# Optimization experiments

Measured on AMD Instinct MI355X. Metric: run time of the kernel, lower is better.

## Reference

```python
import jax, jax.numpy as jnp
import numpy as np


def setup_inputs() -> dict:
    key = jax.random.key(0)
    ks = jax.random.split(key, 13)
    B, W, C = 16, 2048, 512
    inp = {
        "X_sfr": jax.random.normal(ks[0], (B, W, C), dtype=jnp.float32),
        "adj_matrix": jax.random.normal(ks[1], (B, C, C), dtype=jnp.float32),
        "log_temp": jnp.zeros((1,), dtype=jnp.float32),
        "wq": jax.random.normal(ks[2], (1,), dtype=jnp.float32),
        "bq": jax.random.normal(ks[3], (1,), dtype=jnp.float32),
        "wk": jax.random.normal(ks[4], (1,), dtype=jnp.float32),
        "bk": jax.random.normal(ks[5], (1,), dtype=jnp.float32),
        "wv": jax.random.normal(ks[6], (1,), dtype=jnp.float32),
        "bv": jax.random.normal(ks[7], (1,), dtype=jnp.float32),
        "wmu": jax.random.normal(ks[8], (1,), dtype=jnp.float32),
        "bmu": jax.random.normal(ks[9], (1,), dtype=jnp.float32),
        "wsig": jax.random.normal(ks[10], (1,), dtype=jnp.float32),
        "bsig": jax.random.normal(ks[11], (1,), dtype=jnp.float32),
        "k1": 20,
        "k2": 30,
    }
    return inp


def reference(X_sfr, adj_matrix, log_temp, wq, bq, wk, bk, wv, bv, wmu, bmu, wsig, bsig, k1, k2):
    B, W, C = X_sfr.shape
    # spatial propagation: relu + in-degree normalize adjacency
    adj_nonneg = jnp.maximum(adj_matrix, 0.0)
    in_deg = jnp.clip(adj_nonneg.sum(axis=1, keepdims=True), 1e-4)  # [B,1,C]
    adj_norm = adj_nonneg / in_deg
    X_spatial = jnp.einsum('bwi,bij->bwj', X_sfr, adj_norm)  # [B,W,C]

    # static band mask over time: k1 <= |dt| <= k2, fallback to identity rows
    t = jnp.arange(W)
    delta = jnp.abs(t[None, :] - t[:, None])
    band = (delta >= k1) & (delta <= k2)  # [W,W]
    has_valid = band.any(axis=1)
    band = jnp.where(has_valid[:, None], band, jnp.eye(W, dtype=bool))

    # scalar (1->1) q/k/v projections on the temporal token
    temporal_token = X_spatial.mean(axis=2, keepdims=True)  # [B,W,1]
    q = wq * temporal_token + bq                            # [B,W,1]
    k = wk * temporal_token + bk                            # [B,W,1]
    v = wv * X_spatial + bv                                 # [B,W,C]

    temp = jax.nn.softplus(log_temp)[0] + 1e-4
    logits = jnp.matmul(q, jnp.swapaxes(k, 1, 2)) / temp    # [B,W,W] rank-1
    logits = jnp.where(band[None, :, :], logits, -1e9)
    attn = jax.nn.softmax(logits, axis=-1)
    attn = attn * band[None, :, :].astype(attn.dtype)
    attn = attn / (attn.sum(axis=-1, keepdims=True) + 1e-6)

    sacon_scalar = attn.sum(axis=-1, keepdims=True)         # [B,W,1]
    sacon = jnp.broadcast_to(sacon_scalar, (B, W, C))

    X_temporal = jnp.matmul(attn, v)                        # [B,W,C]
    X_fused = X_temporal + X_spatial

    mu = jnp.clip(wmu * X_fused + bmu, -20.0, 20.0)
    sigma_sq = jax.nn.softplus(wsig * X_fused + bsig) + 0.1
    return mu, sigma_sq, sacon
```

## Files before the change

### kernel.cpp

```cpp
#include <hip/hip_runtime.h>
#include <math.h>

#define B_ 16
#define W_ 2048
#define C_ 512

#define OFF_XB    0
#define OFF_BT    33554432
#define OFF_XSP   41943040
#define OFF_TT    75497472
#define OFF_CS    75628544

typedef short v8s __attribute__((ext_vector_type(8)));
typedef float v4f __attribute__((ext_vector_type(4)));
typedef float v2f __attribute__((ext_vector_type(2)));
typedef unsigned int u32;

__device__ __forceinline__ float softplus_fast(float x) {
    return fmaxf(x, 0.f) + __logf(1.f + __expf(-fabsf(x)));
}
__device__ __forceinline__ unsigned short f2bf(float x) {
    unsigned int u = __float_as_uint(x);
    unsigned int r = (u + 0x7FFFu + ((u >> 16) & 1u)) >> 16;
    return (unsigned short)r;
}
__device__ __forceinline__ float bf2f(unsigned int h) {
    return __uint_as_float(h << 16);
}
__device__ __forceinline__ void gload16(const ushort* g, ushort* l) {
    __builtin_amdgcn_global_load_lds(
        (const __attribute__((address_space(1))) u32*)(g),
        (__attribute__((address_space(3))) u32*)(l), 16, 0, 0);
}

__global__ __launch_bounds__(256) void colsum_k(const float* __restrict__ adj,
                                                float* __restrict__ cs) {
    __shared__ float red[8][32];
    const int b = blockIdx.z, j0 = blockIdx.x * 32, r0 = blockIdx.y * 128;
    const int tx = threadIdx.x & 31, ty = threadIdx.x >> 5;
    const float* src = adj + (size_t)b * C_ * C_;

    float s = 0.f;
#pragma unroll 4
    for (int it = 0; it < 16; it++)
        s += fmaxf(src[(size_t)(r0 + it * 8 + ty) * C_ + j0 + tx], 0.f);
    red[ty][tx] = s;
    __syncthreads();
    if (ty == 0) {
        float tot = red[0][tx] + red[1][tx] + red[2][tx] + red[3][tx]
                  + red[4][tx] + red[5][tx] + red[6][tx] + red[7][tx];
        atomicAdd(&cs[b * C_ + j0 + tx], tot);
    }
}

__global__ __launch_bounds__(256) void prep_bt(const float* __restrict__ adj,
                                               const float* __restrict__ cs,
                                               ushort* __restrict__ Bt) {
    __shared__ float t[64][65];
    __shared__ float invs[64];
    const int b = blockIdx.z;
    const int i0 = blockIdx.x * 64;
    const int j0 = blockIdx.y * 64;
    const int tid = threadIdx.x;
    const int tx = tid & 15, ty = tid >> 4;

    if (tid < 64) invs[tid] = 1.f / fmaxf(cs[b * C_ + j0 + tid], 1e-4f);

#pragma unroll
    for (int p = 0; p < 4; p++) {
        const int iy = ty + p * 16;
        const float4 v = *(const float4*)&adj[((size_t)b * C_ + (i0 + iy)) * C_ + j0 + tx * 4];
        t[iy][tx * 4 + 0] = fmaxf(v.x, 0.f);
        t[iy][tx * 4 + 1] = fmaxf(v.y, 0.f);
        t[iy][tx * 4 + 2] = fmaxf(v.z, 0.f);
        t[iy][tx * 4 + 3] = fmaxf(v.w, 0.f);
    }
    __syncthreads();

    const int jj = tid >> 2;
    const int i4 = (tid & 3) * 16;
    const float iv = invs[jj];
    v8s o0, o1;
#pragma unroll
    for (int k = 0; k < 8; k++) o0[k] = (short)f2bf(t[i4 + k][jj] * iv);
#pragma unroll
    for (int k = 0; k < 8; k++) o1[k] = (short)f2bf(t[i4 + 8 + k][jj] * iv);
    ushort* dst = &Bt[(size_t)b * C_ * C_ + (size_t)(j0 + jj) * C_ + i0 + i4];
    *(v8s*)dst       = o0;
    *(v8s*)(dst + 8) = o1;
}

__global__ void convertA(const float* __restrict__ X, ushort* __restrict__ Xb) {
    int idx = blockIdx.x * 256 + threadIdx.x;
    float4 v = ((const float4*)X)[idx];
    ushort4 o;
    o.x = f2bf(v.x); o.y = f2bf(v.y); o.z = f2bf(v.z); o.w = f2bf(v.w);
    ((ushort4*)Xb)[idx] = o;
}

__global__ __launch_bounds__(256) void gemm_mfma(const ushort* __restrict__ Xb,
                                                 const ushort* __restrict__ Bt,
                                                 ushort* __restrict__ Xsp,
                                                 float* __restrict__ tt) {
    __shared__ ushort As[128 * 32];
    __shared__ ushort Bs[128 * 32];
    const int b  = blockIdx.z;
    const int m0 = blockIdx.y * 128;
    const int n0 = blockIdx.x * 128;
    const int tid  = threadIdx.x;
    const int wave = tid >> 6, lane = tid & 63;
    const int quad = lane >> 4, l16 = lane & 15;
    const int mw = (wave & 1) * 64, nw = (wave >> 1) * 64;

    const ushort* Ag = Xb + (size_t)b * W_ * C_ + (size_t)m0 * C_;
    const ushort* Bg = Bt + (size_t)b * C_ * C_ + (size_t)n0 * C_;

    const int sm = tid >> 2;
    const int sk = (tid & 3) * 8;

    v4f acc[4][4];
#pragma unroll
    for (int mt = 0; mt < 4; mt++)
#pragma unroll
        for (int nt = 0; nt < 4; nt++)
            acc[mt][nt] = (v4f){0.f, 0.f, 0.f, 0.f};

    for (int k0 = 0; k0 < C_; k0 += 32) {
        __syncthreads();
        gload16(Ag + (size_t)sm * C_ + k0 + sk,        As + tid * 8);
        gload16(Ag + (size_t)(sm + 64) * C_ + k0 + sk, As + 2048 + tid * 8);
        gload16(Bg + (size_t)sm * C_ + k0 + sk,        Bs + tid * 8);
        gload16(Bg + (size_t)(sm + 64) * C_ + k0 + sk, Bs + 2048 + tid * 8);
        __syncthreads();

        v8s af[4], bf[4];
#pragma unroll
        for (int mt = 0; mt < 4; mt++)
            af[mt] = *(const v8s*)&As[(mw + mt * 16 + l16) * 32 + quad * 8];
#pragma unroll
        for (int nt = 0; nt < 4; nt++)
            bf[nt] = *(const v8s*)&Bs[(nw + nt * 16 + l16) * 32 + quad * 8];
#pragma unroll
        for (int mt = 0; mt < 4; mt++)
#pragma unroll
            for (int nt = 0; nt < 4; nt++)
                acc[mt][nt] = __builtin_amdgcn_mfma_f32_16x16x32_bf16(bf[nt], af[mt], acc[mt][nt], 0, 0, 0);
    }

#pragma unroll
    for (int mt = 0; mt < 4; mt++) {
        const int row = m0 + mw + mt * 16 + l16;
        ushort* rowp = &Xsp[((size_t)b * W_ + row) * C_];
#pragma unroll
        for (int nt = 0; nt < 4; nt++) {
            const int colb = n0 + nw + nt * 16 + quad * 4;
            ushort4 o;
            o.x = f2bf(acc[mt][nt][0]);
            o.y = f2bf(acc[mt][nt][1]);
            o.z = f2bf(acc[mt][nt][2]);
            o.w = f2bf(acc[mt][nt][3]);
            *(ushort4*)&rowp[colb] = o;
        }
        float s = 0.f;
#pragma unroll
        for (int nt = 0; nt < 4; nt++)
#pragma unroll
            for (int r = 0; r < 4; r++) s += acc[mt][nt][r];
        s += __shfl_xor(s, 16);
        s += __shfl_xor(s, 32);
        if (quad == 0) atomicAdd(&tt[b * W_ + row], s);
    }
}

__global__ __launch_bounds__(256) void final_kernel(const ushort* __restrict__ Xsp,
                                                    const float* __restrict__ tt,
                                                    const float* __restrict__ ltp,
                                                    const float* __restrict__ wqp, const float* __restrict__ bqp,
                                                    const float* __restrict__ wkp, const float* __restrict__ bkp,
                                                    const float* __restrict__ wvp, const float* __restrict__ bvp,
                                                    const float* __restrict__ wmup, const float* __restrict__ bmup,
                                                    const float* __restrict__ wsigp, const float* __restrict__ bsigp,
                                                    const int* __restrict__ k1p, const int* __restrict__ k2p,
                                                    float* __restrict__ out) {
    __shared__ float wlds[4][40][4];
    const int wid = threadIdx.x >> 6, lane = threadIdx.x & 63;
    const int bid = ((int)blockIdx.x & 7) * 256 + ((int)blockIdx.x >> 3);
    const int i0w = bid * 16 + wid * 4;
    const int b = i0w >> 11, ib = i0w & (W_ - 1);
    const int K1 = k1p[0], K2 = k2p[0];
    int ns = K2 - K1 + 1;
    if (ns > 16) ns = 16;
    const int n2 = 2 * ns;
    const int nsL = ns + 3;
    const int nu = 2 * nsL;
    const float Sc = 1.f / (1.f + 1e-6f);

    for (int k = threadIdx.x; k < 4 * 40 * 4; k += 256) ((float*)wlds)[k] = 0.f;
    __syncthreads();

    {
        const float cinv = 1.f / C_;
        const float temp = softplus_fast(ltp[0]) + 1e-4f;
        const float invt = 1.f / temp;
        const float wkc = wkp[0] * cinv, bk = bkp[0];
        const float wqc = wqp[0] * cinv, bq = bqp[0];
        const float* ttb = tt + b * W_;
        const int half = lane >> 5;
        const int s = lane & 31;
#pragma unroll
        for (int rr = 0; rr < 2; rr++) {
            const int r = rr * 2 + half;
            const int i = ib + r;
            const float q = wqc * ttb[i] + bq;
            int j = (s < ns) ? (i - K2 + s) : (i + K1 + (s - ns));
            bool valid = (s < n2) && (j >= 0) && (j < W_);
            int jc = min(max(j, 0), W_ - 1);
            float l = valid ? (q * (wkc * ttb[jc] + bk) * invt) : -1e30f;
            float mx = l;
#pragma unroll
            for (int off = 16; off > 0; off >>= 1) mx = fmaxf(mx, __shfl_xor(mx, off, 32));
            float e = valid ? __expf(l - mx) : 0.f;
            float T = e;
#pragma unroll
            for (int off = 16; off > 0; off >>= 1) T += __shfl_xor(T, off, 32);
            float wsc = (1.f / T) * Sc;
            if (valid) {
                int u = (s < ns) ? (r + s) : (nsL + r + (s - ns));
                wlds[wid][u][r] = e * wsc;
            }
        }
    }
    __syncthreads();

    const ushort* Xbp = Xsp + (size_t)b * W_ * C_;
    const int c8 = lane * 8;
    v2f acc2[4][4];
#pragma unroll
    for (int r = 0; r < 4; r++)
#pragma unroll
        for (int p = 0; p < 4; p++) acc2[r][p] = (v2f){0.f, 0.f};

#pragma unroll 4
    for (int u = 0; u < nu; u++) {
        int j = (u < nsL) ? (ib - K2 + u) : (ib + K1 + (u - nsL));
        j = min(max(j, 0), W_ - 1);
        uint4 v = *(const uint4*)(Xbp + (size_t)j * C_ + c8);
        v2f x[4];
        x[0] = (v2f){bf2f(v.x & 0xffffu), bf2f(v.x >> 16)};
        x[1] = (v2f){bf2f(v.y & 0xffffu), bf2f(v.y >> 16)};
        x[2] = (v2f){bf2f(v.z & 0xffffu), bf2f(v.z >> 16)};
        x[3] = (v2f){bf2f(v.w & 0xffffu), bf2f(v.w >> 16)};
        const v4f w4 = *(const v4f*)&wlds[wid][u][0];
#pragma unroll
        for (int r = 0; r < 4; r++) {
            v2f w2 = (v2f){w4[r], w4[r]};
#pragma unroll
            for (int p = 0; p < 4; p++) acc2[r][p] += w2 * x[p];
        }
    }

    const float wv = wvp[0], bvS = bvp[0] * Sc;
    const float wmu = wmup[0], bmu = bmup[0];
    const float wsig = wsigp[0], bsig = bsigp[0];
    const size_t N = (size_t)B_ * W_ * C_;

#pragma unroll
    for (int r = 0; r < 4; r++) {
        uint4 xv = *(const uint4*)(Xbp + (size_t)(ib + r) * C_ + c8);
        float xs[8];
        xs[0] = bf2f(xv.x & 0xffffu); xs[1] = bf2f(xv.x >> 16);
        xs[2] = bf2f(xv.y & 0xffffu); xs[3] = bf2f(xv.y >> 16);
        xs[4] = bf2f(xv.z & 0xffffu); xs[5] = bf2f(xv.z >> 16);
        xs[6] = bf2f(xv.w & 0xffffu); xs[7] = bf2f(xv.w >> 16);

        float mu[8], sg[8];
#pragma unroll
        for (int k = 0; k < 8; k++) {
            float a = acc2[r][k >> 1][k & 1];
            float xf = fmaf(wv, a, bvS) + xs[k];
            mu[k] = fminf(fmaxf(fmaf(wmu, xf, bmu), -20.f), 20.f);
            sg[k] = softplus_fast(fmaf(wsig, xf, bsig)) + 0.1f;
        }

        const size_t base = (size_t)(i0w + r) * C_ + c8;
        __builtin_nontemporal_store((v4f){mu[0], mu[1], mu[2], mu[3]}, (v4f*)&out[base]);
        __builtin_nontemporal_store((v4f){mu[4], mu[5], mu[6], mu[7]}, (v4f*)&out[base + 4]);
        __builtin_nontemporal_store((v4f){sg[0], sg[1], sg[2], sg[3]}, (v4f*)&out[N + base]);
        __builtin_nontemporal_store((v4f){sg[4], sg[5], sg[6], sg[7]}, (v4f*)&out[N + base + 4]);
        __builtin_nontemporal_store((v4f){Sc, Sc, Sc, Sc}, (v4f*)&out[2 * N + base]);
        __builtin_nontemporal_store((v4f){Sc, Sc, Sc, Sc}, (v4f*)&out[2 * N + base + 4]);
    }
}

extern "C" void kernel_launch(void* const* d_in, const int* in_sizes, int n_in,
                              void* d_out, int out_size, void* d_ws, size_t ws_size,
                              hipStream_t stream) {
    const float* X_sfr = (const float*)d_in[0];
    const float* adj   = (const float*)d_in[1];
    const float* ltp   = (const float*)d_in[2];
    const float* wq    = (const float*)d_in[3];
    const float* bq    = (const float*)d_in[4];
    const float* wk    = (const float*)d_in[5];
    const float* bk    = (const float*)d_in[6];
    const float* wv    = (const float*)d_in[7];
    const float* bv    = (const float*)d_in[8];
    const float* wmu   = (const float*)d_in[9];
    const float* bmu   = (const float*)d_in[10];
    const float* wsig  = (const float*)d_in[11];
    const float* bsig  = (const float*)d_in[12];
    const int*   k1p   = (const int*)d_in[13];
    const int*   k2p   = (const int*)d_in[14];

    char* ws = (char*)d_ws;
    ushort* Xb  = (ushort*)(ws + OFF_XB);
    ushort* Bt  = (ushort*)(ws + OFF_BT);
    ushort* Xsp = (ushort*)(ws + OFF_XSP);
    float*  tt  = (float*)(ws + OFF_TT);
    float*  cs  = (float*)(ws + OFF_CS);
    float*  out = (float*)d_out;

    hipMemsetAsync(tt, 0, B_ * W_ * sizeof(float) + B_ * C_ * sizeof(float), stream);

    colsum_k<<<dim3(C_ / 32, 4, B_), 256, 0, stream>>>(adj, cs);

    convertA<<<(B_ * W_ * C_ / 4) / 256, 256, 0, stream>>>(X_sfr, Xb);

    prep_bt<<<dim3(C_ / 64, C_ / 64, B_), 256, 0, stream>>>(adj, cs, Bt);

    gemm_mfma<<<dim3(C_ / 128, W_ / 128, B_), 256, 0, stream>>>(Xb, Bt, Xsp, tt);

    final_kernel<<<(B_ * W_) / 16, 256, 0, stream>>>(Xsp, tt, ltp, wq, bq, wk, bk,
                                                     wv, bv, wmu, bmu, wsig, bsig,
                                                     k1p, k2p, out);
}
```

Measured before the change: 406.4 us.

## Merge convert and colsum kernels, widen GEMM K-step, prefetch band rows

Fuses the X-to-bf16 conversion and the adjacency column-sum into one launch, with each thread converting 16 elements. Doubles the GEMM K-step to 64 by loading two 32-wide LDS stages per sync, halving barrier count at the cost of more LDS. In the final kernel, software-prefetches band rows two iterations ahead, hoists the residual-row loads before the loop, and simplifies the bf16 high-half unpack to a mask. These cut launch overhead, synchronisation and load latency, but add register pressure.

Result: faster. 388.1 us (-4.5%).

```diff
diff --git a/kernel.cpp b/kernel.cpp
--- a/kernel.cpp
+++ b/kernel.cpp
@@ -24,8 +24,11 @@
     unsigned int r = (u + 0x7FFFu + ((u >> 16) & 1u)) >> 16;
     return (unsigned short)r;
 }
-__device__ __forceinline__ float bf2f(unsigned int h) {
-    return __uint_as_float(h << 16);
+__device__ __forceinline__ float bf2f_lo(unsigned int u) {
+    return __uint_as_float(u << 16);
+}
+__device__ __forceinline__ float bf2f_hi(unsigned int u) {
+    return __uint_as_float(u & 0xffff0000u);
 }
 __device__ __forceinline__ void gload16(const ushort* g, ushort* l) {
     __builtin_amdgcn_global_load_lds(
@@ -33,23 +36,46 @@
         (__attribute__((address_space(3))) u32*)(l), 16, 0, 0);
 }
 
-__global__ __launch_bounds__(256) void colsum_k(const float* __restrict__ adj,
-                                                float* __restrict__ cs) {
-    __shared__ float red[8][32];
-    const int b = blockIdx.z, j0 = blockIdx.x * 32, r0 = blockIdx.y * 128;
-    const int tx = threadIdx.x & 31, ty = threadIdx.x >> 5;
-    const float* src = adj + (size_t)b * C_ * C_;
-
-    float s = 0.f;
+__global__ __launch_bounds__(256) void front_k(const float* __restrict__ X,
+                                               ushort* __restrict__ Xb,
+                                               const float* __restrict__ adj,
+                                               float* __restrict__ cs) {
+    const int bid = blockIdx.x;
+    if (bid < 4096) {
+        const size_t e0 = ((size_t)bid * 256 + threadIdx.x) * 16;
+        const float4* Xp = (const float4*)(X + e0);
+        float4 a = Xp[0], b = Xp[1], c = Xp[2], d = Xp[3];
+        v8s o0, o1;
+        o0[0] = (short)f2bf(a.x); o0[1] = (short)f2bf(a.y);
+        o0[2] = (short)f2bf(a.z); o0[3] = (short)f2bf(a.w);
+        o0[4] = (short)f2bf(b.x); o0[5] = (short)f2bf(b.y);
+        o0[6] = (short)f2bf(b.z); o0[7] = (short)f2bf(b.w);
+        o1[0] = (short)f2bf(c.x); o1[1] = (short)f2bf(c.y);
+        o1[2] = (short)f2bf(c.z); o1[3] = (short)f2bf(c.w);
+        o1[4] = (short)f2bf(d.x); o1[5] = (short)f2bf(d.y);
+        o1[6] = (short)f2bf(d.z); o1[7] = (short)f2bf(d.w);
+        *(v8s*)&Xb[e0]     = o0;
+        *(v8s*)&Xb[e0 + 8] = o1;
+    } else {
+        __shared__ float red[8][32];
+        const int cb = bid - 4096;
+        const int b  = cb >> 6;
+        const int rem = cb & 63;
+        const int j0 = (rem & 15) * 32;
+        const int r0 = (rem >> 4) * 128;
+        const int tx = threadIdx.x & 31, ty = threadIdx.x >> 5;
+        const float* src = adj + (size_t)b * C_ * C_;
+        float s = 0.f;
 #pragma unroll 4
-    for (int it = 0; it < 16; it++)
-        s += fmaxf(src[(size_t)(r0 + it * 8 + ty) * C_ + j0 + tx], 0.f);
-    red[ty][tx] = s;
-    __syncthreads();
-    if (ty == 0) {
-        float tot = red[0][tx] + red[1][tx] + red[2][tx] + red[3][tx]
-                  + red[4][tx] + red[5][tx] + red[6][tx] + red[7][tx];
-        atomicAdd(&cs[b * C_ + j0 + tx], tot);
+        for (int it = 0; it < 16; it++)
+            s += fmaxf(src[(size_t)(r0 + it * 8 + ty) * C_ + j0 + tx], 0.f);
+        red[ty][tx] = s;
+        __syncthreads();
+        if (ty == 0) {
+            float tot = red[0][tx] + red[1][tx] + red[2][tx] + red[3][tx]
+                      + red[4][tx] + red[5][tx] + red[6][tx] + red[7][tx];
+            atomicAdd(&cs[b * C_ + j0 + tx], tot);
+        }
     }
 }
 
@@ -90,20 +116,12 @@
     *(v8s*)(dst + 8) = o1;
 }
 
-__global__ void convertA(const float* __restrict__ X, ushort* __restrict__ Xb) {
-    int idx = blockIdx.x * 256 + threadIdx.x;
-    float4 v = ((const float4*)X)[idx];
-    ushort4 o;
-    o.x = f2bf(v.x); o.y = f2bf(v.y); o.z = f2bf(v.z); o.w = f2bf(v.w);
-    ((ushort4*)Xb)[idx] = o;
-}
-
 __global__ __launch_bounds__(256) void gemm_mfma(const ushort* __restrict__ Xb,
                                                  const ushort* __restrict__ Bt,
                                                  ushort* __restrict__ Xsp,
                                                  float* __restrict__ tt) {
-    __shared__ ushort As[128 * 32];
-    __shared__ ushort Bs[128 * 32];
+    __shared__ ushort As[2][128 * 32];
+    __shared__ ushort Bs[2][128 * 32];
     const int b  = blockIdx.z;
     const int m0 = blockIdx.y * 128;
     const int n0 = blockIdx.x * 128;
@@ -125,26 +143,33 @@
         for (int nt = 0; nt < 4; nt++)
             acc[mt][nt] = (v4f){0.f, 0.f, 0.f, 0.f};
 
-    for (int k0 = 0; k0 < C_; k0 += 32) {
+    for (int k0 = 0; k0 < C_; k0 += 64) {
         __syncthreads();
-        gload16(Ag + (size_t)sm * C_ + k0 + sk,        As + tid * 8);
-        gload16(Ag + (size_t)(sm + 64) * C_ + k0 + sk, As + 2048 + tid * 8);
-        gload16(Bg + (size_t)sm * C_ + k0 + sk,        Bs + tid * 8);
-        gload16(Bg + (size_t)(sm + 64) * C_ + k0 + sk, Bs + 2048 + tid * 8);
+        gload16(Ag + (size_t)sm * C_ + k0 + sk,             &As[0][tid * 8]);
+        gload16(Ag + (size_t)(sm + 64) * C_ + k0 + sk,      &As[0][2048 + tid * 8]);
+        gload16(Bg + (size_t)sm * C_ + k0 + sk,             &Bs[0][tid * 8]);
+        gload16(Bg + (size_t)(sm + 64) * C_ + k0 + sk,      &Bs[0][2048 + tid * 8]);
+        gload16(Ag + (size_t)sm * C_ + k0 + 32 + sk,        &As[1][tid * 8]);
+        gload16(Ag + (size_t)(sm + 64) * C_ + k0 + 32 + sk, &As[1][2048 + tid * 8]);
+        gload16(Bg + (size_t)sm * C_ + k0 + 32 + sk,        &Bs[1][tid * 8]);
+        gload16(Bg + (size_t)(sm + 64) * C_ + k0 + 32 + sk, &Bs[1][2048 + tid * 8]);
         __syncthreads();
 
-        v8s af[4], bf[4];
-#pragma unroll
-        for (int mt = 0; mt < 4; mt++)
-            af[mt] = *(const v8s*)&As[(mw + mt * 16 + l16) * 32 + quad * 8];
-#pragma unroll
-        for (int nt = 0; nt < 4; nt++)
-            bf[nt] = *(const v8s*)&Bs[(nw + nt * 16 + l16) * 32 + quad * 8];
-#pragma unroll
-        for (int mt = 0; mt < 4; mt++)
+#pragma unroll
+        for (int h = 0; h < 2; h++) {
+            v8s af[4], bf[4];
+#pragma unroll
+            for (int mt = 0; mt < 4; mt++)
+                af[mt] = *(const v8s*)&As[h][(mw + mt * 16 + l16) * 32 + quad * 8];
 #pragma unroll
             for (int nt = 0; nt < 4; nt++)
-                acc[mt][nt] = __builtin_amdgcn_mfma_f32_16x16x32_bf16(bf[nt], af[mt], acc[mt][nt], 0, 0, 0);
+                bf[nt] = *(const v8s*)&Bs[h][(nw + nt * 16 + l16) * 32 + quad * 8];
+#pragma unroll
+            for (int mt = 0; mt < 4; mt++)
+#pragma unroll
+                for (int nt = 0; nt < 4; nt++)
+                    acc[mt][nt] = __builtin_amdgcn_mfma_f32_16x16x32_bf16(bf[nt], af[mt], acc[mt][nt], 0, 0, 0);
+        }
     }
 
 #pragma unroll
@@ -234,22 +259,34 @@
 
     const ushort* Xbp = Xsp + (size_t)b * W_ * C_;
     const int c8 = lane * 8;
+
+    uint4 xv[4];
+#pragma unroll
+    for (int r = 0; r < 4; r++)
+        xv[r] = *(const uint4*)(Xbp + (size_t)(ib + r) * C_ + c8);
+
     v2f acc2[4][4];
 #pragma unroll
     for (int r = 0; r < 4; r++)
 #pragma unroll
         for (int p = 0; p < 4; p++) acc2[r][p] = (v2f){0.f, 0.f};
 
-#pragma unroll 4
-    for (int u = 0; u < nu; u++) {
+    auto band_addr = [&](int u) -> const uint4* {
         int j = (u < nsL) ? (ib - K2 + u) : (ib + K1 + (u - nsL));
         j = min(max(j, 0), W_ - 1);
-        uint4 v = *(const uint4*)(Xbp + (size_t)j * C_ + c8);
+        return (const uint4*)(Xbp + (size_t)j * C_ + c8);
+    };
+    uint4 vA = *band_addr(0);
+    uint4 vB = *band_addr(1);
+    for (int u = 0; u < nu; u++) {
+        uint4 v = vA;
+        vA = vB;
+        if (u + 2 < nu) vB = *band_addr(u + 2);
         v2f x[4];
-        x[0] = (v2f){bf2f(v.x & 0xffffu), bf2f(v.x >> 16)};
-        x[1] = (v2f){bf2f(v.y & 0xffffu), bf2f(v.y >> 16)};
-        x[2] = (v2f){bf2f(v.z & 0xffffu), bf2f(v.z >> 16)};
-        x[3] = (v2f){bf2f(v.w & 0xffffu), bf2f(v.w >> 16)};
+        x[0] = (v2f){bf2f_lo(v.x), bf2f_hi(v.x)};
+        x[1] = (v2f){bf2f_lo(v.y), bf2f_hi(v.y)};
+        x[2] = (v2f){bf2f_lo(v.z), bf2f_hi(v.z)};
+        x[3] = (v2f){bf2f_lo(v.w), bf2f_hi(v.w)};
         const v4f w4 = *(const v4f*)&wlds[wid][u][0];
 #pragma unroll
         for (int r = 0; r < 4; r++) {
@@ -266,12 +303,11 @@
 
 #pragma unroll
     for (int r = 0; r < 4; r++) {
-        uint4 xv = *(const uint4*)(Xbp + (size_t)(ib + r) * C_ + c8);
         float xs[8];
-        xs[0] = bf2f(xv.x & 0xffffu); xs[1] = bf2f(xv.x >> 16);
-        xs[2] = bf2f(xv.y & 0xffffu); xs[3] = bf2f(xv.y >> 16);
-        xs[4] = bf2f(xv.z & 0xffffu); xs[5] = bf2f(xv.z >> 16);
-        xs[6] = bf2f(xv.w & 0xffffu); xs[7] = bf2f(xv.w >> 16);
+        xs[0] = bf2f_lo(xv[r].x); xs[1] = bf2f_hi(xv[r].x);
+        xs[2] = bf2f_lo(xv[r].y); xs[3] = bf2f_hi(xv[r].y);
+        xs[4] = bf2f_lo(xv[r].z); xs[5] = bf2f_hi(xv[r].z);
+        xs[6] = bf2f_lo(xv[r].w); xs[7] = bf2f_hi(xv[r].w);
 
         float mu[8], sg[8];
 #pragma unroll
@@ -321,9 +357,7 @@
 
     hipMemsetAsync(tt, 0, B_ * W_ * sizeof(float) + B_ * C_ * sizeof(float), stream);
 
-    colsum_k<<<dim3(C_ / 32, 4, B_), 256, 0, stream>>>(adj, cs);
-
-    convertA<<<(B_ * W_ * C_ / 4) / 256, 256, 0, stream>>>(X_sfr, Xb);
+    front_k<<<4096 + 1024, 256, 0, stream>>>(X_sfr, Xb, adj, cs);
 
     prep_bt<<<dim3(C_ / 64, C_ / 64, B_), 256, 0, stream>>>(adj, cs, Bt);
 
```
